# Kernel optimization log

Hardware: AMD Instinct MI355X
Metric: run time of the kernel (lower is better)

Reference implementation:

```python
import jax, jax.numpy as jnp
import numpy as np

B, N, D, H = 4, 2048, 512, 8
KD = D // H  # per-head key/value dim = 64
NORM = 1.0 / np.sqrt(KD).astype(np.float32)


def setup_inputs() -> dict:
    key = jax.random.key(0)
    kq, km, k1, k2, k3 = jax.random.split(key, 5)
    s = 1.0 / np.sqrt(D)
    return {
        "queries": jax.random.normal(kq, (B, N, D), dtype=jnp.float32),
        "mask": jax.random.randint(km, (B, N, N), 0, 2).astype(jnp.bool_),
        "Wq": jax.random.normal(k1, (D, D), dtype=jnp.float32) * s,
        "Wk": jax.random.normal(k2, (D, D), dtype=jnp.float32) * s,
        "Wc": jax.random.normal(k3, (D, D), dtype=jnp.float32) * s,
    }


def reference(queries, mask, Wq, Wk, Wc):
    # Self-attention path (keys=None, values=None): V uses key_embed (Wk).
    Q = (queries @ Wq.T).reshape(B, N, H, KD)  # [B,N,H,kd]
    K = (queries @ Wk.T).reshape(B, N, H, KD)
    V = K  # original code: V = key_embed(queries) when values is None
    scores = NORM * jnp.einsum("bqhd,bkhd->bhqk", Q, K)  # [B,H,N,N]
    scores = jnp.where(mask[:, None, :, :], -jnp.inf, scores)
    attn = jax.nn.softmax(scores, axis=-1)
    out = jnp.einsum("bhqk,bkhd->bqhd", attn, V).reshape(B, N, H * KD)
    return out @ Wc.T  # [B,N,D]
```

## Files before the change

kernel.cpp:

```cpp
#include <hip/hip_runtime.h>
#include <hip/hip_bf16.h>
#include <math.h>

#define B_ 4
#define N_ 2048
#define D_ 512
#define H_ 8
#define NORM2_ 0.18033688011112042f

typedef __attribute__((ext_vector_type(8))) short short8;
typedef __attribute__((ext_vector_type(4))) float f32x4;
#define MFMA16(a, b, c) __builtin_amdgcn_mfma_f32_16x16x32_bf16(a, b, c, 0, 0, 0)
#define EXP2(x) __builtin_amdgcn_exp2f(x)

static __device__ __forceinline__ uint32_t pk2(float lo, float hi) {
  __hip_bfloat162 h = __float22bfloat162_rn(make_float2(lo, hi));
  return *(reinterpret_cast<uint32_t*>(&h));
}

static __device__ __forceinline__ void async16(const ushort* lds, const ushort* g) {
  __builtin_amdgcn_global_load_lds(
      (const __attribute__((address_space(1))) uint32_t*)g,
      (__attribute__((address_space(3))) uint32_t*)(ushort*)lds, 16, 0, 0);
}

__global__ __launch_bounds__(256) void prep(const float* __restrict__ q,
                                            const int* __restrict__ mask,
                                            const float* __restrict__ wq,
                                            const float* __restrict__ wk,
                                            const float* __restrict__ wc,
                                            ushort* __restrict__ Xb,
                                            ushort* __restrict__ Wb,
                                            uint32_t* __restrict__ mb) {
  const int bx = blockIdx.x;
  if (bx < 2048) {
    const int gid = (bx << 8) + threadIdx.x;
    for (int i = gid; i < 4194304; i += 524288) {
      const int4 m = ((const int4*)mask)[i];
      const uint32_t v = (m.x ? 0u : 0xFFu) | (m.y ? 0u : 0xFF00u) |
                         (m.z ? 0u : 0xFF0000u) | (m.w ? 0u : 0xFF000000u);
      mb[i] = v;
    }
  } else if (bx < 3072) {
    const int i = ((bx - 2048) << 8) + threadIdx.x;
    for (int j = i; j < 1048576; j += 262144) {
      const float4 v = ((const float4*)q)[j];
      uint2 o; o.x = pk2(v.x, v.y); o.y = pk2(v.z, v.w);
      ((uint2*)Xb)[j] = o;
    }
  } else {
    const int i = ((bx - 3072) << 8) + threadIdx.x;
    for (int j = i; j < 196608; j += 24576) {
      const int wi = j >> 16, off = j & 65535;
      const float* src = (wi == 0) ? wq : (wi == 1) ? wk : wc;
      const float4 v = ((const float4*)src)[off];
      uint2 o; o.x = pk2(v.x, v.y); o.y = pk2(v.z, v.w);
      ((uint2*)Wb)[j] = o;
    }
  }
}

template <int F32OUT>
__global__ __launch_bounds__(256) void gemm128(const ushort* __restrict__ X,
                                               const ushort* __restrict__ W0,
                                               const ushort* __restrict__ W1,
                                               void* __restrict__ C0,
                                               void* __restrict__ C1,
                                               float s0, float s1) {
  const ushort* Wp = (blockIdx.z == 0) ? W0 : W1;
  void* Cp = (blockIdx.z == 0) ? C0 : C1;
  const float sc = (blockIdx.z == 0) ? s0 : s1;
  const int t = threadIdx.x;
  const int w = t >> 6, lane = t & 63, quad = lane >> 4, c = lane & 15;
  const int wm = w & 1, wn = w >> 1;
  const int n0 = blockIdx.x * 128, m0 = blockIdx.y * 128;
  __shared__ __align__(16) ushort Xs[128][64];
  __shared__ __align__(16) ushort Ws[128][64];
  f32x4 acc[4][4];
#pragma unroll
  for (int i = 0; i < 4; ++i)
#pragma unroll
    for (int j = 0; j < 4; ++j) acc[i][j] = (f32x4){0.f, 0.f, 0.f, 0.f};

  for (int k0 = 0; k0 < D_; k0 += 64) {
    __syncthreads();
#pragma unroll
    for (int g = 0; g < 4; ++g) {
      const int id = w * 256 + g * 64 + lane;
      const int row = id >> 3, lch = id & 7;
      const int gch = lch ^ (row & 7);
      async16(&Xs[row][lch * 8], X + (size_t)(m0 + row) * D_ + k0 + gch * 8);
      async16(&Ws[row][lch * 8], Wp + (size_t)(n0 + row) * D_ + k0 + gch * 8);
    }
    __syncthreads();
#pragma unroll
    for (int s = 0; s < 2; ++s) {
      short8 af[4], bt[4];
#pragma unroll
      for (int i = 0; i < 4; ++i) {
        const int rA = wn * 64 + i * 16 + c;
        af[i] = *(const short8*)&Ws[rA][(((s * 4 + quad) ^ (rA & 7)) & 7) * 8];
        const int rB = wm * 64 + i * 16 + c;
        bt[i] = *(const short8*)&Xs[rB][(((s * 4 + quad) ^ (rB & 7)) & 7) * 8];
      }
#pragma unroll
      for (int i = 0; i < 4; ++i)
#pragma unroll
        for (int j = 0; j < 4; ++j) acc[i][j] = MFMA16(af[i], bt[j], acc[i][j]);
    }
  }
#pragma unroll
  for (int i = 0; i < 4; ++i)
#pragma unroll
    for (int j = 0; j < 4; ++j) {
      const size_t off =
          (size_t)(m0 + wm * 64 + j * 16 + c) * D_ + n0 + wn * 64 + i * 16 + quad * 4;
      if (F32OUT) {
        float4 v; v.x = acc[i][j][0]; v.y = acc[i][j][1]; v.z = acc[i][j][2]; v.w = acc[i][j][3];
        *(float4*)((float*)Cp + off) = v;
      } else {
        uint2 uv;
        uv.x = pk2(acc[i][j][0] * sc, acc[i][j][1] * sc);
        uv.y = pk2(acc[i][j][2] * sc, acc[i][j][3] * sc);
        *(uint2*)((ushort*)Cp + off) = uv;
      }
    }
}

__global__ __launch_bounds__(256) void attn_mfma(const ushort* __restrict__ Qb,
                                                 const ushort* __restrict__ Kb,
                                                 const unsigned char* __restrict__ mb,
                                                 ushort* __restrict__ Ab) {
  const int Lx = blockIdx.x;
  const int wk = ((Lx & 7) << 7) | (Lx >> 3);
  const int h = wk & 7, qt64 = (wk >> 3) & 31, b = wk >> 8;
  const int q0 = qt64 * 64;
  const int t = threadIdx.x;
  const int w = t >> 6, lane = t & 63, quad = lane >> 4, c = lane & 15;

  __shared__ __align__(16) ushort Ks[64][64];
  __shared__ __align__(16) uint32_t KtU[64][32];
  __shared__ __align__(16) ushort QP[4][16][72];
  ushort(*Qs)[64] = (ushort(*)[64]) & QP[0][0][0];
  ushort(*Pq)[16][72] = QP;

#pragma unroll
  for (int p = 0; p < 2; ++p) {
    const int id = t + p * 256;
    const int row = id >> 3, lch = id & 7, gch = lch ^ (row & 7);
    async16(&Qs[row][lch * 8], Qb + (size_t)(b * N_ + q0 + row) * D_ + h * 64 + gch * 8);
  }
  __syncthreads();
  const int rq = (w << 4) + c;
  const short8 bq0 = *(const short8*)&Qs[rq][((quad ^ (rq & 7)) & 7) * 8];
  const short8 bq1 = *(const short8*)&Qs[rq][(((4 + quad) ^ (rq & 7)) & 7) * 8];

  short8 vones;
#pragma unroll
  for (int i = 0; i < 8; ++i) vones[i] = (short)0x3F80;

  f32x4 o[4];
#pragma unroll
  for (int i = 0; i < 4; ++i) o[i] = (f32x4){0.f, 0.f, 0.f, 0.f};
  f32x4 o5 = (f32x4){0.f, 0.f, 0.f, 0.f};

  const int kp = t >> 3, ch = t & 7;
  const int r0 = 2 * kp, r1 = r0 + 1;
  const int ksw0 = ((ch ^ (r0 & 7)) & 7) * 8, ksw1 = ((ch ^ (r1 & 7)) & 7) * 8;
  const ushort* kb0 = Kb + (size_t)(b * N_ + 2 * kp) * D_ + h * 64 + ch * 8;
  const uint32_t* mrow =
      (const uint32_t*)(mb + (size_t)(b * N_ + q0 + (w << 4) + c) * N_) + quad;

  uint4 c0 = *(const uint4*)kb0;
  uint4 c1 = *(const uint4*)(kb0 + D_);
  uint32_t cm[4], nxm[4];
#pragma unroll
  for (int tI = 0; tI < 4; ++tI) cm[tI] = mrow[(tI & 1) * 4 + (tI >> 1) * 8];
  uint4 nx0, nx1;

  const int NT = N_ / 64;
  for (int kt = 0; kt < NT; ++kt) {
    __syncthreads();
    *(uint4*)&Ks[r0][ksw0] = c0;
    *(uint4*)&Ks[r1][ksw1] = c1;
    const uint32_t* a0 = (const uint32_t*)&c0;
    const uint32_t* a1 = (const uint32_t*)&c1;
#pragma unroll
    for (int m = 0; m < 4; ++m) {
      const uint32_t lo = __builtin_amdgcn_perm(a1[m], a0[m], 0x05040100);
      const uint32_t hi = __builtin_amdgcn_perm(a1[m], a0[m], 0x07060302);
      const int j0 = 2 * m, j1 = 2 * m + 1;
      KtU[ch * 8 + j0][(kp & 3) | ((((kp >> 2) ^ j0 ^ ch) & 7) << 2)] = lo;
      KtU[ch * 8 + j1][(kp & 3) | ((((kp >> 2) ^ j1 ^ ch) & 7) << 2)] = hi;
    }
    __syncthreads();

    if (kt + 1 < NT) {
      const ushort* kbn = kb0 + (size_t)(kt + 1) * 64 * D_;
      nx0 = *(const uint4*)kbn;
      nx1 = *(const uint4*)(kbn + D_);
#pragma unroll
      for (int tI = 0; tI < 4; ++tI)
        nxm[tI] = mrow[(kt + 1) * 16 + (tI & 1) * 4 + (tI >> 1) * 8];
    }

#pragma unroll
    for (int tI = 0; tI < 4; ++tI) {
      const int rk = tI * 16 + c;
      const short8 aK0 = *(const short8*)&Ks[rk][((quad ^ (rk & 7)) & 7) * 8];
      const short8 aK1 = *(const short8*)&Ks[rk][(((4 + quad) ^ (rk & 7)) & 7) * 8];
      f32x4 z = (f32x4){0.f, 0.f, 0.f, 0.f};
      z = MFMA16(aK0, bq0, z);
      z = MFMA16(aK1, bq1, z);
      const uint32_t mw = cm[tI];
      const uint32_t mlo = __builtin_amdgcn_perm(mw, mw, 0x01010000);
      const uint32_t mhi = __builtin_amdgcn_perm(mw, mw, 0x03030202);
      uint32_t pb[4];
#pragma unroll
      for (int r = 0; r < 4; ++r) pb[r] = __float_as_uint(EXP2(z[r]));
      const uint32_t pw0 = __builtin_amdgcn_perm(pb[1], pb[0], 0x07060302) & mlo;
      const uint32_t pw1 = __builtin_amdgcn_perm(pb[3], pb[2], 0x07060302) & mhi;
      *(uint2*)&Pq[w][c][tI * 16 + quad * 4] = make_uint2(pw0, pw1);
    }

    const short8 bp0 = *(const short8*)&Pq[w][c][quad * 8];
    const short8 bp1 = *(const short8*)&Pq[w][c][32 + quad * 8];
    __builtin_amdgcn_s_setprio(1);
    o5 = MFMA16(vones, bp0, o5);
    o5 = MFMA16(vones, bp1, o5);
#pragma unroll
    for (int dt = 0; dt < 4; ++dt) {
      const int dd = dt * 16 + c;
      const int g = (c & 7) ^ ((2 * dt + (c >> 3)) & 7);
      const short8 aV0 = *(const short8*)&KtU[dd][((quad ^ g) & 7) << 2];
      const short8 aV1 = *(const short8*)&KtU[dd][(((4 + quad) ^ g) & 7) << 2];
      o[dt] = MFMA16(aV0, bp0, o[dt]);
      o[dt] = MFMA16(aV1, bp1, o[dt]);
    }
    __builtin_amdgcn_s_setprio(0);

    if (kt + 1 < NT) {
      c0 = nx0; c1 = nx1;
#pragma unroll
      for (int tI = 0; tI < 4; ++tI) cm[tI] = nxm[tI];
    }
  }

  const float inv = 1.f / o5[0];
#pragma unroll
  for (int dt = 0; dt < 4; ++dt) {
    uint2 uv;
    uv.x = pk2(o[dt][0] * inv, o[dt][1] * inv);
    uv.y = pk2(o[dt][2] * inv, o[dt][3] * inv);
    *(uint2*)(Ab + (size_t)(b * N_ + q0 + (w << 4) + c) * D_ + h * 64 + dt * 16 + quad * 4) = uv;
  }
}

extern "C" void kernel_launch(void* const* d_in, const int* in_sizes, int n_in,
                              void* d_out, int out_size, void* d_ws, size_t ws_size,
                              hipStream_t stream) {
  const float* queries = (const float*)d_in[0];
  const int* mask = (const int*)d_in[1];
  const float* Wq = (const float*)d_in[2];
  const float* Wk = (const float*)d_in[3];
  const float* Wc = (const float*)d_in[4];
  float* out = (float*)d_out;

  const size_t nTok = (size_t)B_ * N_;
  const size_t nXD = nTok * D_;
  const size_t nW = (size_t)D_ * D_;
  ushort* Xb = (ushort*)d_ws;
  ushort* Wqb = Xb + nXD;
  ushort* Wkb = Wqb + nW;
  ushort* Wcb = Wkb + nW;
  ushort* Qb = Wcb + nW;
  ushort* Kb = Qb + nXD;
  ushort* Ab = Kb + nXD;
  uint32_t* mb = (uint32_t*)(Ab + nXD);

  prep<<<3168, 256, 0, stream>>>(queries, mask, Wq, Wk, Wc, Xb, Wqb, mb);
  gemm128<0><<<dim3(D_ / 128, (int)(nTok / 128), 2), 256, 0, stream>>>(
      Xb, Wqb, Wkb, Qb, Kb, NORM2_, 1.0f);
  attn_mfma<<<dim3(N_ / 64 * H_ * B_), 256, 0, stream>>>(
      Qb, Kb, (const unsigned char*)mb, Ab);
  gemm128<1><<<dim3(D_ / 128, (int)(nTok / 128), 1), 256, 0, stream>>>(
      Ab, Wcb, nullptr, out, nullptr, 1.0f, 1.0f);
}
```

Baseline: 224.4 us.

## Double-buffer K and transposed-K LDS tiles to drop one barrier per iteration

Ks and KtU become ping-pong LDS buffers. The next tile is staged into the alternate buffer while the current one is consumed, so each key-tile iteration needs one __syncthreads instead of two. Global prefetch of K now runs two tiles ahead, and the s_setprio hints around the PV MFMAs are removed. LDS usage roughly doubles for K, which may reduce occupancy, and the extra live registers for the two-ahead prefetch add register pressure.

```diff
diff --git a/kernel.cpp b/kernel.cpp
--- a/kernel.cpp
+++ b/kernel.cpp
@@ -138,8 +138,8 @@
   const int t = threadIdx.x;
   const int w = t >> 6, lane = t & 63, quad = lane >> 4, c = lane & 15;
 
-  __shared__ __align__(16) ushort Ks[64][64];
-  __shared__ __align__(16) uint32_t KtU[64][32];
+  __shared__ __align__(16) ushort Ks[2][64][64];
+  __shared__ __align__(16) uint32_t KtU[2][64][32];
   __shared__ __align__(16) ushort QP[4][16][72];
   ushort(*Qs)[64] = (ushort(*)[64]) & QP[0][0][0];
   ushort(*Pq)[16][72] = QP;
@@ -150,19 +150,6 @@
     const int row = id >> 3, lch = id & 7, gch = lch ^ (row & 7);
     async16(&Qs[row][lch * 8], Qb + (size_t)(b * N_ + q0 + row) * D_ + h * 64 + gch * 8);
   }
-  __syncthreads();
-  const int rq = (w << 4) + c;
-  const short8 bq0 = *(const short8*)&Qs[rq][((quad ^ (rq & 7)) & 7) * 8];
-  const short8 bq1 = *(const short8*)&Qs[rq][(((4 + quad) ^ (rq & 7)) & 7) * 8];
-
-  short8 vones;
-#pragma unroll
-  for (int i = 0; i < 8; ++i) vones[i] = (short)0x3F80;
-
-  f32x4 o[4];
-#pragma unroll
-  for (int i = 0; i < 4; ++i) o[i] = (f32x4){0.f, 0.f, 0.f, 0.f};
-  f32x4 o5 = (f32x4){0.f, 0.f, 0.f, 0.f};
 
   const int kp = t >> 3, ch = t & 7;
   const int r0 = 2 * kp, r1 = r0 + 1;
@@ -176,29 +163,55 @@
   uint32_t cm[4], nxm[4];
 #pragma unroll
   for (int tI = 0; tI < 4; ++tI) cm[tI] = mrow[(tI & 1) * 4 + (tI >> 1) * 8];
+  __syncthreads();
+
+  const int rq = (w << 4) + c;
+  const short8 bq0 = *(const short8*)&Qs[rq][((quad ^ (rq & 7)) & 7) * 8];
+  const short8 bq1 = *(const short8*)&Qs[rq][(((4 + quad) ^ (rq & 7)) & 7) * 8];
+
+#define STAGE(bf)                                                               \
+  do {                                                                          \
+    *(uint4*)&Ks[bf][r0][ksw0] = c0;                                            \
+    *(uint4*)&Ks[bf][r1][ksw1] = c1;                                            \
+    const uint32_t* a0 = (const uint32_t*)&c0;                                  \
+    const uint32_t* a1 = (const uint32_t*)&c1;                                  \
+    _Pragma("unroll") for (int m = 0; m < 4; ++m) {                             \
+      const uint32_t lo = __builtin_amdgcn_perm(a1[m], a0[m], 0x05040100);      \
+      const uint32_t hi = __builtin_amdgcn_perm(a1[m], a0[m], 0x07060302);      \
+      const int j0 = 2 * m, j1 = 2 * m + 1;                                     \
+      KtU[bf][ch * 8 + j0][(kp & 3) | ((((kp >> 2) ^ j0 ^ ch) & 7) << 2)] = lo; \
+      KtU[bf][ch * 8 + j1][(kp & 3) | ((((kp >> 2) ^ j1 ^ ch) & 7) << 2)] = hi; \
+    }                                                                           \
+  } while (0)
+
+  STAGE(0);
+  {
+    const ushort* kbn = kb0 + (size_t)64 * D_;
+    c0 = *(const uint4*)kbn;
+    c1 = *(const uint4*)(kbn + D_);
+  }
+
+  short8 vones;
+#pragma unroll
+  for (int i = 0; i < 8; ++i) vones[i] = (short)0x3F80;
+
+  f32x4 o[4];
+#pragma unroll
+  for (int i = 0; i < 4; ++i) o[i] = (f32x4){0.f, 0.f, 0.f, 0.f};
+  f32x4 o5 = (f32x4){0.f, 0.f, 0.f, 0.f};
+
   uint4 nx0, nx1;
-
   const int NT = N_ / 64;
   for (int kt = 0; kt < NT; ++kt) {
+    const int p = kt & 1;
     __syncthreads();
-    *(uint4*)&Ks[r0][ksw0] = c0;
-    *(uint4*)&Ks[r1][ksw1] = c1;
-    const uint32_t* a0 = (const uint32_t*)&c0;
-    const uint32_t* a1 = (const uint32_t*)&c1;
-#pragma unroll
-    for (int m = 0; m < 4; ++m) {
-      const uint32_t lo = __builtin_amdgcn_perm(a1[m], a0[m], 0x05040100);
-      const uint32_t hi = __builtin_amdgcn_perm(a1[m], a0[m], 0x07060302);
-      const int j0 = 2 * m, j1 = 2 * m + 1;
-      KtU[ch * 8 + j0][(kp & 3) | ((((kp >> 2) ^ j0 ^ ch) & 7) << 2)] = lo;
-      KtU[ch * 8 + j1][(kp & 3) | ((((kp >> 2) ^ j1 ^ ch) & 7) << 2)] = hi;
-    }
-    __syncthreads();
-
-    if (kt + 1 < NT) {
-      const ushort* kbn = kb0 + (size_t)(kt + 1) * 64 * D_;
+    if (kt + 1 < NT) STAGE(p ^ 1);
+    if (kt + 2 < NT) {
+      const ushort* kbn = kb0 + (size_t)(kt + 2) * 64 * D_;
       nx0 = *(const uint4*)kbn;
       nx1 = *(const uint4*)(kbn + D_);
+    }
+    if (kt + 1 < NT) {
 #pragma unroll
       for (int tI = 0; tI < 4; ++tI)
         nxm[tI] = mrow[(kt + 1) * 16 + (tI & 1) * 4 + (tI >> 1) * 8];
@@ -207,8 +220,8 @@
 #pragma unroll
     for (int tI = 0; tI < 4; ++tI) {
       const int rk = tI * 16 + c;
-      const short8 aK0 = *(const short8*)&Ks[rk][((quad ^ (rk & 7)) & 7) * 8];
-      const short8 aK1 = *(const short8*)&Ks[rk][(((4 + quad) ^ (rk & 7)) & 7) * 8];
+      const short8 aK0 = *(const short8*)&Ks[p][rk][((quad ^ (rk & 7)) & 7) * 8];
+      const short8 aK1 = *(const short8*)&Ks[p][rk][(((4 + quad) ^ (rk & 7)) & 7) * 8];
       f32x4 z = (f32x4){0.f, 0.f, 0.f, 0.f};
       z = MFMA16(aK0, bq0, z);
       z = MFMA16(aK1, bq1, z);
@@ -225,26 +238,25 @@
 
     const short8 bp0 = *(const short8*)&Pq[w][c][quad * 8];
     const short8 bp1 = *(const short8*)&Pq[w][c][32 + quad * 8];
-    __builtin_amdgcn_s_setprio(1);
     o5 = MFMA16(vones, bp0, o5);
     o5 = MFMA16(vones, bp1, o5);
 #pragma unroll
     for (int dt = 0; dt < 4; ++dt) {
       const int dd = dt * 16 + c;
       const int g = (c & 7) ^ ((2 * dt + (c >> 3)) & 7);
-      const short8 aV0 = *(const short8*)&KtU[dd][((quad ^ g) & 7) << 2];
-      const short8 aV1 = *(const short8*)&KtU[dd][(((4 + quad) ^ g) & 7) << 2];
+      const short8 aV0 = *(const short8*)&KtU[p][dd][((quad ^ g) & 7) << 2];
+      const short8 aV1 = *(const short8*)&KtU[p][dd][(((4 + quad) ^ g) & 7) << 2];
       o[dt] = MFMA16(aV0, bp0, o[dt]);
       o[dt] = MFMA16(aV1, bp1, o[dt]);
     }
-    __builtin_amdgcn_s_setprio(0);
-
+
+    if (kt + 2 < NT) { c0 = nx0; c1 = nx1; }
     if (kt + 1 < NT) {
-      c0 = nx0; c1 = nx1;
 #pragma unroll
       for (int tI = 0; tI < 4; ++tI) cm[tI] = nxm[tI];
     }
   }
+#undef STAGE
 
   const float inv = 1.f / o5[0];
 #pragma unroll
```

After: 248.2 us. 10.6% more time.
